# Kernel tuning notes

Hardware: AMD Instinct MI355X
Metric: run time of the kernel (lower is better)

Reference implementation:

```python
import jax, jax.numpy as jnp
import numpy as np

N_NODES = 100000
N_EDGES = 1600000
HIDDEN = 128
VOCAB = 2048


def setup_inputs() -> dict:
    key = jax.random.key(0)
    k1, k2, k3, k4 = jax.random.split(key, 4)
    x = jax.random.normal(k1, (N_NODES, HIDDEN), dtype=jnp.float32)
    edge_index = jax.random.randint(k2, (2, N_EDGES), 0, N_NODES, dtype=jnp.int64)
    # torch Linear default init ~ U(-1/sqrt(fan_in), 1/sqrt(fan_in)); scale randn similarly
    W_trn = jax.random.normal(k3, (HIDDEN, HIDDEN), dtype=jnp.float32) / np.sqrt(HIDDEN)
    b_trn = jnp.zeros((HIDDEN,), dtype=jnp.float32)
    W_prd = jax.random.normal(k4, (HIDDEN, VOCAB), dtype=jnp.float32) / np.sqrt(HIDDEN)
    b_prd = jnp.zeros((VOCAB,), dtype=jnp.float32)
    return {"x": x, "edge_index": edge_index, "W_trn": W_trn, "b_trn": b_trn,
            "W_prd": W_prd, "b_prd": b_prd}


def reference(x, edge_index, W_trn, b_trn, W_prd, b_prd):
    # GINConv(nn=Identity, eps=0): out[i] = x[i] + sum_{j -> i} x[j]
    src = edge_index[0]  # message sources
    dst = edge_index[1]  # aggregation targets
    agg = jax.ops.segment_sum(x[src], dst, num_segments=x.shape[0])  # [N, H]
    h = x + agg
    h = h @ W_trn + b_trn          # [N, H]
    logits = h @ W_prd + b_prd     # [N, vocab]
    return logits
```

## Files before the change

### kernel.cpp

```cpp
#include <hip/hip_runtime.h>
#include <hip/hip_bf16.h>

#define HIDDEN 128
#define VOCAB  2048
#define CAP    128

using frag_ab = __attribute__((ext_vector_type(8))) short;
using frag_cd = __attribute__((ext_vector_type(4))) float;

static __device__ __forceinline__ unsigned short f2bf(float f) {
    __hip_bfloat16 b = __float2bfloat16(f);
    return *reinterpret_cast<unsigned short*>(&b);
}
static __device__ __forceinline__ float bflo(unsigned int w) {
    return __uint_as_float(w << 16);
}
static __device__ __forceinline__ float bfhi(unsigned int w) {
    return __uint_as_float(w & 0xffff0000u);
}

__global__ void prep_kernel(const float* __restrict__ Wt,
                            const float* __restrict__ Wp,
                            const float* __restrict__ bt,
                            const float* __restrict__ bp,
                            const float4* __restrict__ x4,
                            unsigned short* __restrict__ wfT,
                            float* __restrict__ bfv,
                            int* __restrict__ deg,
                            uint2* __restrict__ xb4,
                            int M, int gM)
{
    int b = blockIdx.x;
    int tid = threadIdx.x;
    if (b < 1024) {
        int gid = b * 256 + tid;
        int n = gid & 2047;
        int k = gid >> 11;
        float acc = 0.f;
#pragma unroll 8
        for (int j = 0; j < 128; ++j)
            acc += Wt[k * 128 + j] * Wp[j * 2048 + n];
        wfT[n * 128 + k] = f2bf(acc);
    } else if (b < 1032) {
        int n = (b - 1024) * 256 + tid;
        float acc = bp[n];
#pragma unroll 8
        for (int j = 0; j < 128; ++j)
            acc += bt[j] * Wp[j * 2048 + n];
        bfv[n] = acc;
    } else if (b < 1032 + gM) {
        int i = (b - 1032) * 256 + tid;
        if (i < M) deg[i] = 0;
    } else {
        int i = (b - 1032 - gM) * 256 + tid;
        int n4 = M * 32;
        if (i < n4) {
            float4 v = x4[i];
            uint2 o;
            o.x = (unsigned int)f2bf(v.x) | ((unsigned int)f2bf(v.y) << 16);
            o.y = (unsigned int)f2bf(v.z) | ((unsigned int)f2bf(v.w) << 16);
            xb4[i] = o;
        }
    }
}

__global__ void bucket_fill_kernel(const int* __restrict__ ei,
                                   int* __restrict__ deg,
                                   int* __restrict__ srclist, int n_edges)
{
    int e = blockIdx.x * 256 + threadIdx.x;
    if (e < n_edges) {
        int d = ei[n_edges + e];
        int pos = atomicAdd(&deg[d], 1);
        if (pos < CAP)
            srclist[(size_t)d * CAP + pos] = ei[e];
    }
}

__global__ void gather_kernel(const unsigned int* __restrict__ xb2,
                              const int* __restrict__ deg,
                              const int* __restrict__ srclist,
                              unsigned int* __restrict__ hb2, int n)
{
    int t = blockIdx.x * 256 + threadIdx.x;
    int node = t >> 6, l = t & 63;
    if (node >= n) return;
    unsigned int wself = xb2[(size_t)node * 64 + l];
    float ax = bflo(wself), ay = bfhi(wself);
    int len = deg[node];
    size_t base = (size_t)node * CAP;

    int cl = l < len ? l : (len > 0 ? len - 1 : 0);
    int eidx = srclist[base + cl];
    int full = len < 64 ? len : 64;
    for (int e = 0; e < full; e += 8) {
        unsigned int w[8];
#pragma unroll
        for (int j = 0; j < 8; ++j) {
            int ee = e + j; if (ee >= full) ee = full - 1;
            int idx = __shfl(eidx, ee);
            w[j] = xb2[(size_t)idx * 64 + l];
        }
#pragma unroll
        for (int j = 0; j < 8; ++j)
            if (e + j < full) { ax += bflo(w[j]); ay += bfhi(w[j]); }
    }
    for (int e = 64; e < len; e += 8) {
        int idx8[8]; unsigned int w[8];
#pragma unroll
        for (int j = 0; j < 8; ++j) {
            int ee = e + j;
            idx8[j] = srclist[base + (ee < len ? ee : len - 1)];
        }
#pragma unroll
        for (int j = 0; j < 8; ++j)
            w[j] = xb2[(size_t)idx8[j] * 64 + l];
#pragma unroll
        for (int j = 0; j < 8; ++j)
            if (e + j < len) { ax += bflo(w[j]); ay += bfhi(w[j]); }
    }
    unsigned int lo = f2bf(ax), hi = f2bf(ay);
    hb2[(size_t)node * 64 + l] = lo | (hi << 16);
}

__global__ __launch_bounds__(256, 2) void gemm_kernel(
    const unsigned short* __restrict__ hbf,
    const unsigned short* __restrict__ wfT,
    const float* __restrict__ bfv,
    float* __restrict__ out, int M)
{
    int tid  = threadIdx.x;
    int wave = tid >> 6;
    int lane = tid & 63;
    int wm = wave >> 1, wn = wave & 1;
    int brow   = blockIdx.y * 128;
    int cbase0 = blockIdx.x * 512;

    int lr = lane & 15;
    int lk = (lane >> 4) * 8;
    int lq = lk >> 3;

    frag_ab a[4][4];
#pragma unroll
    for (int mi = 0; mi < 4; ++mi) {
        int r = brow + wm * 64 + mi * 16 + lr;
        if (r > M - 1) r = M - 1;
        const frag_ab* p = reinterpret_cast<const frag_ab*>(&hbf[(size_t)r * HIDDEN]);
#pragma unroll
        for (int kk = 0; kk < 4; ++kk)
            a[mi][kk] = p[kk * 4 + lq];
    }

#pragma unroll
    for (int c = 0; c < 4; ++c) {
        int cb = cbase0 + c * 128 + wn * 64;
        frag_cd acc[4][4] = {};
#pragma unroll
        for (int kk = 0; kk < 4; ++kk) {
            frag_ab b[4];
#pragma unroll
            for (int ni = 0; ni < 4; ++ni) {
                int nr = cb + ni * 16 + lr;
                b[ni] = *reinterpret_cast<const frag_ab*>(
                    &wfT[(size_t)nr * HIDDEN + kk * 32 + lk]);
            }
#pragma unroll
            for (int mi = 0; mi < 4; ++mi)
#pragma unroll
                for (int ni = 0; ni < 4; ++ni)
                    acc[mi][ni] = __builtin_amdgcn_mfma_f32_16x16x32_bf16(
                        b[ni], a[mi][kk], acc[mi][ni], 0, 0, 0);
        }

        int nq = (lane >> 4) * 4;
#pragma unroll
        for (int mi = 0; mi < 4; ++mi) {
            int grow = brow + wm * 64 + mi * 16 + lr;
            if (grow >= M) continue;
            size_t ro = (size_t)grow * VOCAB;
#pragma unroll
            for (int ni = 0; ni < 4; ++ni) {
                int gcol = cb + ni * 16 + nq;
                float4 b4 = *reinterpret_cast<const float4*>(&bfv[gcol]);
                float4 o;
                o.x = acc[mi][ni][0] + b4.x;
                o.y = acc[mi][ni][1] + b4.y;
                o.z = acc[mi][ni][2] + b4.z;
                o.w = acc[mi][ni][3] + b4.w;
                *reinterpret_cast<float4*>(&out[ro + gcol]) = o;
            }
        }
    }
}

extern "C" void kernel_launch(void* const* d_in, const int* in_sizes, int n_in,
                              void* d_out, int out_size, void* d_ws, size_t ws_size,
                              hipStream_t stream) {
    const float* x  = (const float*)d_in[0];
    const int*   ei = (const int*)d_in[1];
    const float* Wt = (const float*)d_in[2];
    const float* bt = (const float*)d_in[3];
    const float* Wp = (const float*)d_in[4];
    const float* bp = (const float*)d_in[5];
    float* out = (float*)d_out;

    int M       = in_sizes[0] / HIDDEN;
    int n_edges = in_sizes[1] / 2;

    char* ws = (char*)d_ws;
    size_t off = 0;
    auto alloc = [&](size_t bytes) { char* p = ws + off; off += (bytes + 15) & ~(size_t)15; return p; };
    unsigned short* wfT     = (unsigned short*)alloc((size_t)VOCAB * HIDDEN * 2);
    float*          bfv     = (float*)alloc(VOCAB * 4);
    int*            deg     = (int*)alloc((size_t)M * 4);
    int*            srclist = (int*)alloc((size_t)M * CAP * 4);
    unsigned short* hb      = (unsigned short*)alloc((size_t)M * HIDDEN * 2);
    unsigned short* xb      = (unsigned short*)alloc((size_t)M * HIDDEN * 2);

    int gM = (M + 255) / 256;
    int gC = (M * 32 + 255) / 256;
    prep_kernel<<<1032 + gM + gC, 256, 0, stream>>>(Wt, Wp, bt, bp, (const float4*)x,
                                                    wfT, bfv, deg, (uint2*)xb, M, gM);

    int gE = (n_edges + 255) / 256;
    bucket_fill_kernel<<<gE, 256, 0, stream>>>(ei, deg, srclist, n_edges);

    int gG = (M * 64 + 255) / 256;
    gather_kernel<<<gG, 256, 0, stream>>>((const unsigned int*)xb, deg, srclist,
                                          (unsigned int*)hb, M);

    dim3 grid(VOCAB / 512, (M + 127) / 128);
    gemm_kernel<<<grid, 256, 0, stream>>>(hb, wfT, bfv, out, M);
}
```

Measured before the change: 432.3 us.

## Fuse neighbor gather into GEMM via shared-memory tile of aggregated features

Merges the gather/aggregation kernel into the GEMM kernel. Each block aggregates 128 nodes into an LDS tile (padded stride) and then computes all 2048 output columns from it. This removes the intermediate hb buffer write and read and one launch. Block count falls from about 3100 to about 780, and the gather phase no longer overlaps with MFMA work, so the two phases serialize within each block. Degree is now clamped to CAP.

```diff
diff --git a/kernel.cpp b/kernel.cpp
--- a/kernel.cpp
+++ b/kernel.cpp
@@ -4,6 +4,7 @@
 #define HIDDEN 128
 #define VOCAB  2048
 #define CAP    128
+#define LDT    136
 
 using frag_ab = __attribute__((ext_vector_type(8))) short;
 using frag_cd = __attribute__((ext_vector_type(4))) float;
@@ -77,83 +78,82 @@
     }
 }
 
-__global__ void gather_kernel(const unsigned int* __restrict__ xb2,
-                              const int* __restrict__ deg,
-                              const int* __restrict__ srclist,
-                              unsigned int* __restrict__ hb2, int n)
-{
-    int t = blockIdx.x * 256 + threadIdx.x;
-    int node = t >> 6, l = t & 63;
-    if (node >= n) return;
-    unsigned int wself = xb2[(size_t)node * 64 + l];
-    float ax = bflo(wself), ay = bfhi(wself);
-    int len = deg[node];
-    size_t base = (size_t)node * CAP;
-
-    int cl = l < len ? l : (len > 0 ? len - 1 : 0);
-    int eidx = srclist[base + cl];
-    int full = len < 64 ? len : 64;
-    for (int e = 0; e < full; e += 8) {
-        unsigned int w[8];
-#pragma unroll
-        for (int j = 0; j < 8; ++j) {
-            int ee = e + j; if (ee >= full) ee = full - 1;
-            int idx = __shfl(eidx, ee);
-            w[j] = xb2[(size_t)idx * 64 + l];
-        }
-#pragma unroll
-        for (int j = 0; j < 8; ++j)
-            if (e + j < full) { ax += bflo(w[j]); ay += bfhi(w[j]); }
-    }
-    for (int e = 64; e < len; e += 8) {
-        int idx8[8]; unsigned int w[8];
-#pragma unroll
-        for (int j = 0; j < 8; ++j) {
-            int ee = e + j;
-            idx8[j] = srclist[base + (ee < len ? ee : len - 1)];
-        }
-#pragma unroll
-        for (int j = 0; j < 8; ++j)
-            w[j] = xb2[(size_t)idx8[j] * 64 + l];
-#pragma unroll
-        for (int j = 0; j < 8; ++j)
-            if (e + j < len) { ax += bflo(w[j]); ay += bfhi(w[j]); }
-    }
-    unsigned int lo = f2bf(ax), hi = f2bf(ay);
-    hb2[(size_t)node * 64 + l] = lo | (hi << 16);
-}
-
-__global__ __launch_bounds__(256, 2) void gemm_kernel(
-    const unsigned short* __restrict__ hbf,
+__global__ __launch_bounds__(256, 2) void fused_kernel(
+    const unsigned int* __restrict__ xb2,
+    const int* __restrict__ deg,
+    const int* __restrict__ srclist,
     const unsigned short* __restrict__ wfT,
     const float* __restrict__ bfv,
     float* __restrict__ out, int M)
 {
+    __shared__ unsigned short hs[128 * LDT];
+
     int tid  = threadIdx.x;
     int wave = tid >> 6;
     int lane = tid & 63;
+    int brow = blockIdx.x * 128;
+
+    for (int nd = wave; nd < 128; nd += 4) {
+        int node = brow + nd;
+        unsigned int packed = 0;
+        if (node < M) {
+            unsigned int wself = xb2[(size_t)node * 64 + lane];
+            float ax = bflo(wself), ay = bfhi(wself);
+            int len = deg[node];
+            if (len > CAP) len = CAP;
+            size_t base = (size_t)node * CAP;
+            int cl = lane < len ? lane : (len > 0 ? len - 1 : 0);
+            int eidx = srclist[base + cl];
+            int full = len < 64 ? len : 64;
+            for (int e = 0; e < full; e += 8) {
+                unsigned int w[8];
+#pragma unroll
+                for (int j = 0; j < 8; ++j) {
+                    int ee = e + j; if (ee >= full) ee = full - 1;
+                    int idx = __shfl(eidx, ee);
+                    w[j] = xb2[(size_t)idx * 64 + lane];
+                }
+#pragma unroll
+                for (int j = 0; j < 8; ++j)
+                    if (e + j < full) { ax += bflo(w[j]); ay += bfhi(w[j]); }
+            }
+            for (int e = 64; e < len; e += 8) {
+                int idx8[8]; unsigned int w[8];
+#pragma unroll
+                for (int j = 0; j < 8; ++j) {
+                    int ee = e + j;
+                    idx8[j] = srclist[base + (ee < len ? ee : len - 1)];
+                }
+#pragma unroll
+                for (int j = 0; j < 8; ++j)
+                    w[j] = xb2[(size_t)idx8[j] * 64 + lane];
+#pragma unroll
+                for (int j = 0; j < 8; ++j)
+                    if (e + j < len) { ax += bflo(w[j]); ay += bfhi(w[j]); }
+            }
+            packed = (unsigned int)f2bf(ax) | ((unsigned int)f2bf(ay) << 16);
+        }
+        *reinterpret_cast<unsigned int*>(&hs[nd * LDT + 2 * lane]) = packed;
+    }
+    __syncthreads();
+
     int wm = wave >> 1, wn = wave & 1;
-    int brow   = blockIdx.y * 128;
-    int cbase0 = blockIdx.x * 512;
-
     int lr = lane & 15;
     int lk = (lane >> 4) * 8;
-    int lq = lk >> 3;
 
     frag_ab a[4][4];
 #pragma unroll
     for (int mi = 0; mi < 4; ++mi) {
-        int r = brow + wm * 64 + mi * 16 + lr;
-        if (r > M - 1) r = M - 1;
-        const frag_ab* p = reinterpret_cast<const frag_ab*>(&hbf[(size_t)r * HIDDEN]);
+        int r = wm * 64 + mi * 16 + lr;
 #pragma unroll
         for (int kk = 0; kk < 4; ++kk)
-            a[mi][kk] = p[kk * 4 + lq];
-    }
-
-#pragma unroll
-    for (int c = 0; c < 4; ++c) {
-        int cb = cbase0 + c * 128 + wn * 64;
+            a[mi][kk] = *reinterpret_cast<const frag_ab*>(&hs[r * LDT + kk * 32 + lk]);
+    }
+
+    int nq = (lane >> 4) * 4;
+#pragma unroll
+    for (int c = 0; c < 16; ++c) {
+        int cb = c * 128 + wn * 64;
         frag_cd acc[4][4] = {};
 #pragma unroll
         for (int kk = 0; kk < 4; ++kk) {
@@ -171,8 +171,6 @@
                     acc[mi][ni] = __builtin_amdgcn_mfma_f32_16x16x32_bf16(
                         b[ni], a[mi][kk], acc[mi][ni], 0, 0, 0);
         }
-
-        int nq = (lane >> 4) * 4;
 #pragma unroll
         for (int mi = 0; mi < 4; ++mi) {
             int grow = brow + wm * 64 + mi * 16 + lr;
@@ -214,7 +212,6 @@
     float*          bfv     = (float*)alloc(VOCAB * 4);
     int*            deg     = (int*)alloc((size_t)M * 4);
     int*            srclist = (int*)alloc((size_t)M * CAP * 4);
-    unsigned short* hb      = (unsigned short*)alloc((size_t)M * HIDDEN * 2);
     unsigned short* xb      = (unsigned short*)alloc((size_t)M * HIDDEN * 2);
 
     int gM = (M + 255) / 256;
@@ -225,10 +222,7 @@
     int gE = (n_edges + 255) / 256;
     bucket_fill_kernel<<<gE, 256, 0, stream>>>(ei, deg, srclist, n_edges);
 
-    int gG = (M * 64 + 255) / 256;
-    gather_kernel<<<gG, 256, 0, stream>>>((const unsigned int*)xb, deg, srclist,
-                                          (unsigned int*)hb, M);
-
-    dim3 grid(VOCAB / 512, (M + 127) / 128);
-    gemm_kernel<<<grid, 256, 0, stream>>>(hb, wfT, bfv, out, M);
-}
+    int gF = (M + 127) / 128;
+    fused_kernel<<<gF, 256, 0, stream>>>((const unsigned int*)xb, deg, srclist,
+                                         wfT, bfv, out, M);
+}
```

Measured after the change: 592.9 us. 37.1% more time.
